# Optimization experiments

Measured on AMD Instinct MI355X. Metric: run time of the kernel, lower is better.

## Reference

```python
import jax, jax.numpy as jnp
import numpy as np

B, N, F_IN, H, MH, STEPS = 8192, 9, 15, 128, 256, 4
E_PER = 16
MASK_IDX = jnp.arange(8)  # mask = [True]*8 + [False]


def setup_inputs() -> dict:
    key = jax.random.key(0)
    ks = jax.random.split(key, 24)
    s = 0.05
    inp = {
        "obs": jax.random.normal(ks[0], (B, 135), jnp.float32),
        "edges": jax.random.randint(ks[1], (B, 2, E_PER), 0, N, jnp.int32),
        "enc_W": jax.random.normal(ks[2], (F_IN, H), jnp.float32) * s,
        "enc_b": jax.random.normal(ks[3], (H,), jnp.float32) * s,
        "msg_W1": jax.random.normal(ks[4], (STEPS, 2 * H, MH), jnp.float32) * s,
        "msg_b1": jax.random.normal(ks[5], (STEPS, MH), jnp.float32) * s,
        "msg_W2": jax.random.normal(ks[6], (STEPS, MH, MH), jnp.float32) * s,
        "msg_b2": jax.random.normal(ks[7], (STEPS, MH), jnp.float32) * s,
        "msg_W3": jax.random.normal(ks[8], (STEPS, MH, H), jnp.float32) * s,
        "msg_b3": jax.random.normal(ks[9], (STEPS, H), jnp.float32) * s,
        "gru_Wi": jax.random.normal(ks[10], (STEPS, H, 3 * H), jnp.float32) * s,
        "gru_Wh": jax.random.normal(ks[11], (STEPS, H, 3 * H), jnp.float32) * s,
        "gru_bi": jax.random.normal(ks[12], (STEPS, 3 * H), jnp.float32) * s,
        "gru_bh": jax.random.normal(ks[13], (STEPS, 3 * H), jnp.float32) * s,
        "dec_W1": jax.random.normal(ks[14], (H, MH), jnp.float32) * s,
        "dec_b1": jax.random.normal(ks[15], (MH,), jnp.float32) * s,
        "dec_W2": jax.random.normal(ks[16], (MH, MH), jnp.float32) * s,
        "dec_b2": jax.random.normal(ks[17], (MH,), jnp.float32) * s,
        "dec_W3": jax.random.normal(ks[18], (MH, 1), jnp.float32) * s,
        "dec_b3": jax.random.normal(ks[19], (1,), jnp.float32) * s,
    }
    return inp


def reference(obs, edges, enc_W, enc_b, msg_W1, msg_b1, msg_W2, msg_b2,
              msg_W3, msg_b3, gru_Wi, gru_Wh, gru_bi, gru_bh,
              dec_W1, dec_b1, dec_W2, dec_b2, dec_W3, dec_b3):
    BN = B * N
    x = obs.reshape(BN, F_IN)                       # [B*N, 15]
    x = jnp.tanh(x @ enc_W + enc_b)                 # encoder -> [B*N, H]

    # flatten per-graph edges into a global edge list, then add self-loops
    offsets = (jnp.arange(B, dtype=jnp.int32) * N)[:, None, None]
    eg = edges + offsets                            # [B, 2, 16]
    loops = jnp.arange(BN, dtype=jnp.int32)
    src = jnp.concatenate([eg[:, 0, :].reshape(-1), loops])  # x_j (source)
    dst = jnp.concatenate([eg[:, 1, :].reshape(-1), loops])  # x_i (target)
    deg = jax.ops.segment_sum(jnp.ones_like(dst, dtype=x.dtype), dst,
                              num_segments=BN)      # >=1 due to self-loops

    for s in range(STEPS):
        m = jnp.concatenate([x[dst], x[src]], axis=-1)       # [E, 2H]
        m = jnp.tanh(m @ msg_W1[s] + msg_b1[s])
        m = jnp.tanh(m @ msg_W2[s] + msg_b2[s])
        m = m @ msg_W3[s] + msg_b3[s]                        # [E, H]
        aggr = jax.ops.segment_sum(m, dst, num_segments=BN) / deg[:, None]
        # GRUCell(input=aggr, hidden=x), PyTorch gate order (r, z, n)
        gi = aggr @ gru_Wi[s] + gru_bi[s]
        gh = x @ gru_Wh[s] + gru_bh[s]
        ir, iz, inn = jnp.split(gi, 3, axis=-1)
        hr, hz, hn = jnp.split(gh, 3, axis=-1)
        r = jax.nn.sigmoid(ir + hr)
        z = jax.nn.sigmoid(iz + hz)
        n = jnp.tanh(inn + r * hn)
        x = (1.0 - z) * n + z * x

    d = jnp.tanh(x @ dec_W1 + dec_b1)
    d = jnp.tanh(d @ dec_W2 + dec_b2)
    d = d @ dec_W3 + dec_b3                                  # [B*N, 1]
    out = d.reshape(B, N)
    return out[:, MASK_IDX]                                  # [B, 8]
```

## Files before the change

### kernel.cpp

```cpp
#include <hip/hip_runtime.h>
#include <hip/hip_bf16.h>
#include <math.h>

#define BGR   8192
#define NND   9
#define BN    73728
#define NE    131072
#define ETOT  204800
#define H     128
#define MH    256
#define FIN   15

typedef __bf16 bf16_t;
typedef bf16_t bf16x8 __attribute__((ext_vector_type(8)));
typedef float  f32x4  __attribute__((ext_vector_type(4)));
typedef float  f32x16 __attribute__((ext_vector_type(16)));

__device__ __forceinline__ unsigned short f2bf(float f) {
    unsigned int u = __float_as_uint(f);
    u += 0x7fff + ((u >> 16) & 1);
    return (unsigned short)(u >> 16);
}
__device__ __forceinline__ unsigned int pkbf(float a, float b) {
    union { __hip_bfloat162 h; unsigned int u; } un;
    un.h = __float22bfloat162_rn(make_float2(a, b));
    return un.u;
}
__device__ __forceinline__ bf16x8 as_frag(int4 v) {
    union { int4 i; bf16x8 f; } u; u.i = v; return u.f;
}
__device__ __forceinline__ float fast_tanh(float v) {
    float e = __expf(2.0f * v);
    return 1.0f - __fdividef(2.0f, e + 1.0f);
}
__device__ __forceinline__ int sw16(int m, int k) {
    return m * 256 + ((((k >> 3) ^ (m & 15)) << 3) | (k & 7));
}
__device__ __forceinline__ int sw_off(int m, int k) {
    return m * 256 + ((((k >> 3) ^ (m & 7)) << 3) | (k & 7));
}

__global__ void deg_kernel(const int* __restrict__ edges, float* __restrict__ inv_deg) {
    int g = blockIdx.x * 256 + threadIdx.x;
    if (g >= BGR) return;
    int cnt[NND];
#pragma unroll
    for (int n = 0; n < NND; ++n) cnt[n] = 1;
    for (int j = 0; j < 16; ++j) {
        int d = edges[g * 32 + 16 + j];
#pragma unroll
        for (int n = 0; n < NND; ++n) cnt[n] += (d == n) ? 1 : 0;
    }
#pragma unroll
    for (int n = 0; n < NND; ++n) inv_deg[g * NND + n] = 1.0f / (float)cnt[n];
}

__global__ void enc_kernel(const float* __restrict__ obs, const float* __restrict__ W,
                           const float* __restrict__ b, float* __restrict__ x) {
    int tid = blockIdx.x * 256 + threadIdx.x;
    int i = tid >> 7, h = tid & 127;
    float acc = b[h];
#pragma unroll
    for (int k = 0; k < FIN; ++k) acc += obs[i * FIN + k] * W[k * H + h];
    x[i * H + h] = tanhf(acc);
}

__global__ void wt_kernel(const float* __restrict__ W1, const float* __restrict__ W2,
                          const float* __restrict__ W3, const float* __restrict__ Wi,
                          const float* __restrict__ Wh, const float* __restrict__ dW1,
                          const float* __restrict__ dW2, unsigned short* __restrict__ out) {
    int idx = blockIdx.x * 256 + threadIdx.x;
    float v;
    if (idx < 262144) {
        int s = idx >> 16, r = idx & 65535, n = r >> 8, k = r & 255;
        v = W1[(s << 16) + (k << 8) + n];
    } else if (idx < 524288) {
        int i2 = idx - 262144;
        int s = i2 >> 16, r = i2 & 65535, n = r >> 8, k = r & 255;
        v = W2[(s << 16) + (k << 8) + n];
    } else if (idx < 655360) {
        int i3 = idx - 524288;
        int s = i3 >> 15, r = i3 & 32767, n = r >> 8, k = r & 255;
        v = W3[(s << 15) + (k << 7) + n];
    } else if (idx < 1179648) {
        int i4 = idx - 655360;
        int s = i4 >> 17, rr = i4 & 131071;
        int p = rr >> 8, k = rr & 255;
        int w = p >> 6, rem = p & 63;
        int gate = rem >> 4, c = rem & 15;
        int h = w * 16 + c;
        const int sb = s * 49152;
        if (gate == 0)      v = (k < 128) ? Wi[sb + k * 384 + h]       : Wh[sb + (k - 128) * 384 + h];
        else if (gate == 1) v = (k < 128) ? Wi[sb + k * 384 + 128 + h] : Wh[sb + (k - 128) * 384 + 128 + h];
        else if (gate == 2) v = (k < 128) ? Wi[sb + k * 384 + 256 + h] : 0.f;
        else                v = (k < 128) ? 0.f                        : Wh[sb + (k - 128) * 384 + 256 + h];
    } else if (idx < 1212416) {
        int i5 = idx - 1179648;
        int n = i5 >> 7, k = i5 & 127;
        v = dW1[k * 256 + n];
    } else {
        int i6 = idx - 1212416;
        int n = i6 >> 8, k = i6 & 255;
        v = dW2[k * 256 + n];
    }
    out[idx] = f2bf(v);
}

__global__ __launch_bounds__(512, 4) void msg_mfma(
        const float* __restrict__ x, const int* __restrict__ edges,
        const unsigned short* __restrict__ W1T, const float* __restrict__ b1,
        const unsigned short* __restrict__ W2T, const float* __restrict__ b2,
        const unsigned short* __restrict__ W3T,
        float* __restrict__ aggr) {
    __shared__ unsigned short bufA[64 * 256];
    __shared__ unsigned short bufB[64 * 256];
    __shared__ int sdst[64];
    const int t  = threadIdx.x;
    const int e0 = blockIdx.x * 64;
    const int wv = t >> 6;
    const int ln = t & 63;
    const int l31 = ln & 31;
    const int lh  = ln >> 5;

    if (t < 64) {
        const int eg = e0 + t;
        sdst[t] = (eg < NE) ? ((eg >> 4) * NND + edges[(eg >> 4) * 32 + 16 + (eg & 15)])
                            : (eg - NE);
    }
    {
        const int row  = t >> 2;
        const int q    = t & 3;
        const int e    = row & 63;
        const int side = row >> 6;
        const int eg   = e0 + e;
        int node;
        if (eg < NE) {
            int g = eg >> 4, j = eg & 15;
            node = g * NND + (side ? edges[g * 32 + j] : edges[g * 32 + 16 + j]);
        } else {
            node = eg - NE;
        }
        const float* xs = x + (size_t)node * H + q * 32;
        const int kbase = side * 128 + q * 32;
#pragma unroll
        for (int i = 0; i < 8; ++i) {
            float4 v = *(const float4*)(xs + i * 4);
            uint2 o;
            o.x = pkbf(v.x, v.y); o.y = pkbf(v.z, v.w);
            *(uint2*)(bufA + sw16(e, kbase + i * 4)) = o;
        }
    }
    __syncthreads();

    {
        f32x16 acc0, acc1;
#pragma unroll
        for (int i = 0; i < 16; ++i) { acc0[i] = 0.f; acc1[i] = 0.f; }
        const unsigned short* wp = W1T + (size_t)(wv * 32 + l31) * 256 + lh * 8;
#pragma unroll
        for (int ks = 0; ks < 16; ++ks) {
            const int kk = ks * 16 + lh * 8;
            bf16x8 a0 = as_frag(*(const int4*)(bufA + sw16(l31, kk)));
            bf16x8 a1 = as_frag(*(const int4*)(bufA + sw16(32 + l31, kk)));
            bf16x8 bw = as_frag(*(const int4*)(wp + ks * 16));
            acc0 = __builtin_amdgcn_mfma_f32_32x32x16_bf16(a0, bw, acc0, 0, 0, 0);
            acc1 = __builtin_amdgcn_mfma_f32_32x32x16_bf16(a1, bw, acc1, 0, 0, 0);
        }
        const int n = wv * 32 + l31;
        const float bias = b1[n];
#pragma unroll
        for (int reg = 0; reg < 16; ++reg) {
            const int mrow = (reg & 3) + ((reg >> 2) << 3) + (lh << 2);
            bufB[sw16(mrow, n)]      = f2bf(fast_tanh(acc0[reg] + bias));
            bufB[sw16(32 + mrow, n)] = f2bf(fast_tanh(acc1[reg] + bias));
        }
    }
    __syncthreads();

    {
        f32x16 acc0, acc1;
#pragma unroll
        for (int i = 0; i < 16; ++i) { acc0[i] = 0.f; acc1[i] = 0.f; }
        const unsigned short* wp = W2T + (size_t)(wv * 32 + l31) * 256 + lh * 8;
#pragma unroll
        for (int ks = 0; ks < 16; ++ks) {
            const int kk = ks * 16 + lh * 8;
            bf16x8 a0 = as_frag(*(const int4*)(bufB + sw16(l31, kk)));
            bf16x8 a1 = as_frag(*(const int4*)(bufB + sw16(32 + l31, kk)));
            bf16x8 bw = as_frag(*(const int4*)(wp + ks * 16));
            acc0 = __builtin_amdgcn_mfma_f32_32x32x16_bf16(a0, bw, acc0, 0, 0, 0);
            acc1 = __builtin_amdgcn_mfma_f32_32x32x16_bf16(a1, bw, acc1, 0, 0, 0);
        }
        const int n = wv * 32 + l31;
        const float bias = b2[n];
#pragma unroll
        for (int reg = 0; reg < 16; ++reg) {
            const int mrow = (reg & 3) + ((reg >> 2) << 3) + (lh << 2);
            bufA[sw16(mrow, n)]      = f2bf(fast_tanh(acc0[reg] + bias));
            bufA[sw16(32 + mrow, n)] = f2bf(fast_tanh(acc1[reg] + bias));
        }
    }
    __syncthreads();

    {
        const int mt = wv & 1, nq = wv >> 1;
        const int n = nq * 32 + l31;
        f32x16 acc;
#pragma unroll
        for (int i = 0; i < 16; ++i) acc[i] = 0.f;
        const unsigned short* wp = W3T + (size_t)n * 256 + lh * 8;
#pragma unroll
        for (int ks = 0; ks < 16; ++ks) {
            const int kk = ks * 16 + lh * 8;
            bf16x8 a = as_frag(*(const int4*)(bufA + sw16(mt * 32 + l31, kk)));
            bf16x8 bw = as_frag(*(const int4*)(wp + ks * 16));
            acc = __builtin_amdgcn_mfma_f32_32x32x16_bf16(a, bw, acc, 0, 0, 0);
        }
#pragma unroll
        for (int reg = 0; reg < 16; ++reg) {
            const int m = mt * 32 + (reg & 3) + ((reg >> 2) << 3) + (lh << 2);
            atomicAdd(aggr + (size_t)sdst[m] * H + n, acc[reg]);
        }
    }
}

__global__ __launch_bounds__(512, 4) void gru_mfma(
        float* __restrict__ x, float* __restrict__ aggr, const float* __restrict__ inv_deg,
        const unsigned short* __restrict__ WG, const float* __restrict__ b3m,
        const float* __restrict__ bi, const float* __restrict__ bh) {
    __shared__ unsigned short bufA[64 * 256];
    const int t = threadIdx.x;
    const int n0 = blockIdx.x * 64;
    const int wv = t >> 6, ln = t & 63, lrow = ln & 15, lq = ln >> 4;

    {
        const int m = t >> 3;
        const int q = t & 7;
        const int k0 = q * 32;
        const int node = n0 + m;
        if (q < 4) {
            const float scale = inv_deg[node];
            const float* src = aggr + (size_t)node * H + k0;
#pragma unroll
            for (int i = 0; i < 8; ++i) {
                float4 v = *(const float4*)(src + i * 4);
                const float4 bb = *(const float4*)(b3m + k0 + i * 4);
                v.x = v.x * scale + bb.x; v.y = v.y * scale + bb.y;
                v.z = v.z * scale + bb.z; v.w = v.w * scale + bb.w;
                uint2 o; o.x = pkbf(v.x, v.y); o.y = pkbf(v.z, v.w);
                *(uint2*)(bufA + sw_off(m, k0 + i * 4)) = o;
            }
        } else {
            const float* src = x + (size_t)node * H + (k0 - 128);
#pragma unroll
            for (int i = 0; i < 8; ++i) {
                float4 v = *(const float4*)(src + i * 4);
                uint2 o; o.x = pkbf(v.x, v.y); o.y = pkbf(v.z, v.w);
                *(uint2*)(bufA + sw_off(m, k0 + i * 4)) = o;
            }
        }
    }
    __syncthreads();

    const f32x4 zero = {0.f, 0.f, 0.f, 0.f};
    f32x4 acc[4][4];
#pragma unroll
    for (int i = 0; i < 4; ++i)
#pragma unroll
        for (int j = 0; j < 4; ++j) acc[i][j] = zero;

    const unsigned short* wgp = WG + (size_t)(wv * 64 + lrow) * 256;
#pragma unroll
    for (int kq = 0; kq < 8; ++kq) {
        const int ko = kq * 32 + lq * 8;
        bf16x8 af[4], bfr[4];
#pragma unroll
        for (int tm = 0; tm < 4; ++tm)
            af[tm] = as_frag(*(const int4*)(bufA + sw_off(tm * 16 + lrow, ko)));
#pragma unroll
        for (int g = 0; g < 4; ++g)
            bfr[g] = as_frag(*(const int4*)(wgp + (size_t)g * 16 * 256 + ko));
#pragma unroll
        for (int tm = 0; tm < 4; ++tm)
#pragma unroll
            for (int g = 0; g < 4; ++g)
                acc[tm][g] = __builtin_amdgcn_mfma_f32_16x16x32_bf16(af[tm], bfr[g], acc[tm][g], 0, 0, 0);
    }

    {
        const int h = wv * 16 + lrow;
        const float b_r = bi[h] + bh[h];
        const float b_z = bi[128 + h] + bh[128 + h];
        const float b_n = bi[256 + h];
        const float b_h = bh[256 + h];
#pragma unroll
        for (int tm = 0; tm < 4; ++tm) {
#pragma unroll
            for (int r = 0; r < 4; ++r) {
                const int node = n0 + tm * 16 + lq * 4 + r;
                const float irhr = acc[tm][0][r] + b_r;
                const float izhz = acc[tm][1][r] + b_z;
                const float inn  = acc[tm][2][r] + b_n;
                const float hn   = acc[tm][3][r] + b_h;
                const float rg = 1.f / (1.f + expf(-irhr));
                const float zg = 1.f / (1.f + expf(-izhz));
                const float ng = tanhf(inn + rg * hn);
                const float xo = x[(size_t)node * H + h];
                x[(size_t)node * H + h] = (1.f - zg) * ng + zg * xo;
                aggr[(size_t)node * H + h] = 0.f;
            }
        }
    }
}

__global__ __launch_bounds__(256, 4) void dec_mfma(
        const float* __restrict__ x,
        const unsigned short* __restrict__ W1T, const float* __restrict__ b1,
        const unsigned short* __restrict__ W2T, const float* __restrict__ b2,
        const float* __restrict__ W3, const float* __restrict__ b3,
        float* __restrict__ out) {
    __shared__ unsigned short buf[64 * 256];
    const int t = threadIdx.x;
    const int id0 = blockIdx.x * 64;
    const int wv = t >> 6, ln = t & 63, lrow = ln & 15, lq = ln >> 4;
    const int nbase = wv * 64;

    {
        const int m = t >> 2, q = t & 3;
        const int id = id0 + m;
        const int node = (id >> 3) * NND + (id & 7);
        const float* src = x + (size_t)node * H + q * 32;
#pragma unroll
        for (int i = 0; i < 8; ++i) {
            float4 v = *(const float4*)(src + i * 4);
            uint2 o; o.x = pkbf(v.x, v.y); o.y = pkbf(v.z, v.w);
            *(uint2*)(buf + sw_off(m, q * 32 + i * 4)) = o;
        }
    }
    __syncthreads();

    const f32x4 zero = {0.f, 0.f, 0.f, 0.f};

    {
        f32x4 acc[4][4];
#pragma unroll
        for (int i = 0; i < 4; ++i)
#pragma unroll
            for (int j = 0; j < 4; ++j) acc[i][j] = zero;
#pragma unroll
        for (int kq = 0; kq < 4; ++kq) {
            const int ko = kq * 32 + lq * 8;
            bf16x8 af[4], bfr[4];
#pragma unroll
            for (int tm = 0; tm < 4; ++tm)
                af[tm] = as_frag(*(const int4*)(buf + sw_off(tm * 16 + lrow, ko)));
#pragma unroll
            for (int tn = 0; tn < 4; ++tn)
                bfr[tn] = as_frag(*(const int4*)(W1T + (size_t)(nbase + tn * 16 + lrow) * 128 + ko));
#pragma unroll
            for (int tm = 0; tm < 4; ++tm)
#pragma unroll
                for (int tn = 0; tn < 4; ++tn)
                    acc[tm][tn] = __builtin_amdgcn_mfma_f32_16x16x32_bf16(af[tm], bfr[tn], acc[tm][tn], 0, 0, 0);
        }
        __syncthreads();
#pragma unroll
        for (int tn = 0; tn < 4; ++tn) {
            const int n = nbase + tn * 16 + lrow;
            const float bias = b1[n];
#pragma unroll
            for (int tm = 0; tm < 4; ++tm)
#pragma unroll
                for (int r = 0; r < 4; ++r) {
                    const int m = tm * 16 + lq * 4 + r;
                    buf[sw_off(m, n)] = f2bf(fast_tanh(acc[tm][tn][r] + bias));
                }
        }
    }
    __syncthreads();

    {
        f32x4 acc[4][4];
#pragma unroll
        for (int i = 0; i < 4; ++i)
#pragma unroll
            for (int j = 0; j < 4; ++j) acc[i][j] = zero;
#pragma unroll
        for (int kq = 0; kq < 8; ++kq) {
            const int ko = kq * 32 + lq * 8;
            bf16x8 af[4], bfr[4];
#pragma unroll
            for (int tm = 0; tm < 4; ++tm)
                af[tm] = as_frag(*(const int4*)(buf + sw_off(tm * 16 + lrow, ko)));
#pragma unroll
            for (int tn = 0; tn < 4; ++tn)
                bfr[tn] = as_frag(*(const int4*)(W2T + (size_t)(nbase + tn * 16 + lrow) * 256 + ko));
#pragma unroll
            for (int tm = 0; tm < 4; ++tm)
#pragma unroll
                for (int tn = 0; tn < 4; ++tn)
                    acc[tm][tn] = __builtin_amdgcn_mfma_f32_16x16x32_bf16(af[tm], bfr[tn], acc[tm][tn], 0, 0, 0);
        }
        __syncthreads();
#pragma unroll
        for (int tn = 0; tn < 4; ++tn) {
            const int n = nbase + tn * 16 + lrow;
            const float bias = b2[n];
#pragma unroll
            for (int tm = 0; tm < 4; ++tm)
#pragma unroll
                for (int r = 0; r < 4; ++r) {
                    const int m = tm * 16 + lq * 4 + r;
                    buf[sw_off(m, n)] = f2bf(fast_tanh(acc[tm][tn][r] + bias));
                }
        }
    }
    __syncthreads();

    {
        const int m = t >> 2, p = t & 3;
        float s = 0.f;
#pragma unroll
        for (int i = 0; i < 64; ++i) {
            const int k = p * 64 + i;
            const float a = __uint_as_float((unsigned int)buf[sw_off(m, k)] << 16);
            s += a * W3[k];
        }
        s += __shfl_xor(s, 1);
        s += __shfl_xor(s, 2);
        if (p == 0) out[id0 + m] = s + b3[0];
    }
}

extern "C" void kernel_launch(void* const* d_in, const int* in_sizes, int n_in,
                              void* d_out, int out_size, void* d_ws, size_t ws_size,
                              hipStream_t stream) {
    const float* obs    = (const float*)d_in[0];
    const int*   edges  = (const int*)  d_in[1];
    const float* enc_W  = (const float*)d_in[2];
    const float* enc_b  = (const float*)d_in[3];
    const float* msg_W1 = (const float*)d_in[4];
    const float* msg_b1 = (const float*)d_in[5];
    const float* msg_W2 = (const float*)d_in[6];
    const float* msg_b2 = (const float*)d_in[7];
    const float* msg_W3 = (const float*)d_in[8];
    const float* msg_b3 = (const float*)d_in[9];
    const float* gru_Wi = (const float*)d_in[10];
    const float* gru_Wh = (const float*)d_in[11];
    const float* gru_bi = (const float*)d_in[12];
    const float* gru_bh = (const float*)d_in[13];
    const float* dec_W1 = (const float*)d_in[14];
    const float* dec_b1 = (const float*)d_in[15];
    const float* dec_W2 = (const float*)d_in[16];
    const float* dec_b2 = (const float*)d_in[17];
    const float* dec_W3 = (const float*)d_in[18];
    const float* dec_b3 = (const float*)d_in[19];

    float* x       = (float*)d_ws;
    float* aggr    = x + (size_t)BN * H;
    float* inv_deg = aggr + (size_t)BN * H;
    unsigned short* wbf = (unsigned short*)(inv_deg + BN);

    hipMemsetAsync(aggr, 0, (size_t)BN * H * sizeof(float), stream);
    deg_kernel<<<(BGR + 255) / 256, 256, 0, stream>>>(edges, inv_deg);
    wt_kernel<<<1277952 / 256, 256, 0, stream>>>(msg_W1, msg_W2, msg_W3, gru_Wi, gru_Wh,
                                                 dec_W1, dec_W2, wbf);
    enc_kernel<<<BN * H / 256, 256, 0, stream>>>(obs, enc_W, enc_b, x);

    for (int s = 0; s < 4; ++s) {
        const unsigned short* W1T = wbf + (size_t)s * 65536;
        const unsigned short* W2T = wbf + 262144 + (size_t)s * 65536;
        const unsigned short* W3T = wbf + 524288 + (size_t)s * 32768;
        const unsigned short* WGs = wbf + 655360 + (size_t)s * 131072;
        msg_mfma<<<ETOT / 64, 512, 0, stream>>>(
            x, edges,
            W1T, msg_b1 + (size_t)s * 256,
            W2T, msg_b2 + (size_t)s * 256,
            W3T,
            aggr);
        gru_mfma<<<BN / 64, 512, 0, stream>>>(
            x, aggr, inv_deg, WGs, msg_b3 + (size_t)s * 128,
            gru_bi + (size_t)s * 384, gru_bh + (size_t)s * 384);
    }

    dec_mfma<<<BGR * 8 / 64, 256, 0, stream>>>(
        x, wbf + 1179648, dec_b1, wbf + 1212416, dec_b2, dec_W3, dec_b3, (float*)d_out);
}
```

Baseline: 1.340 ms.

## Precompute per-node first-layer projections before edge gather in message MLP

The first message layer concat(x_dst, x_src) @ W1 is split into per-node projections x@W1_top and x@W1_bot. A new proj_mfma kernel computes them once per node (73,728 nodes rather than 204,800 edges) and stores them in bf16. msg_mfma then gathers the two projections, adds them with the bias, applies tanh, and runs only the second and third layers. This removes about a third of the edge-level MFMA work, at the cost of an extra kernel launch, a bf16 intermediate buffer written and read per step, and extra rounding on the pre-activation.

Measured after the change: 1.351 ms. About the same (+0.8%).

```diff
diff --git a/kernel.cpp b/kernel.cpp
--- a/kernel.cpp
+++ b/kernel.cpp
@@ -35,6 +35,9 @@
 }
 __device__ __forceinline__ int sw16(int m, int k) {
     return m * 256 + ((((k >> 3) ^ (m & 15)) << 3) | (k & 7));
+}
+__device__ __forceinline__ int swp(int m, int k) {
+    return m * 128 + ((((k >> 3) ^ (m & 15)) << 3) | (k & 7));
 }
 __device__ __forceinline__ int sw_off(int m, int k) {
     return m * 256 + ((((k >> 3) ^ (m & 7)) << 3) | (k & 7));
@@ -98,17 +101,80 @@
         int i5 = idx - 1179648;
         int n = i5 >> 7, k = i5 & 127;
         v = dW1[k * 256 + n];
-    } else {
+    } else if (idx < 1277952) {
         int i6 = idx - 1212416;
         int n = i6 >> 8, k = i6 & 255;
         v = dW2[k * 256 + n];
+    } else {
+        int i7 = idx - 1277952;
+        int s = i7 >> 16, rr = i7 & 65535;
+        int n = rr >> 7, k = rr & 127;
+        v = (n < 256) ? W1[(s << 16) + (k << 8) + n]
+                      : W1[(s << 16) + ((k + 128) << 8) + (n - 256)];
     }
     out[idx] = f2bf(v);
 }
 
+__global__ __launch_bounds__(512, 4) void proj_mfma(
+        const float* __restrict__ x, const unsigned short* __restrict__ W1P,
+        unsigned short* __restrict__ P) {
+    __shared__ unsigned short lbuf[64 * 128];
+    const int t = threadIdx.x;
+    const int n0 = blockIdx.x * 64;
+    const int wv = t >> 6, ln = t & 63, l31 = ln & 31, lh = ln >> 5;
+
+    {
+        const int m = t >> 3, q = t & 7;
+        const float* xs = x + (size_t)(n0 + m) * H + q * 16;
+#pragma unroll
+        for (int i = 0; i < 4; ++i) {
+            float4 v = *(const float4*)(xs + i * 4);
+            uint2 o; o.x = pkbf(v.x, v.y); o.y = pkbf(v.z, v.w);
+            *(uint2*)(lbuf + swp(m, q * 16 + i * 4)) = o;
+        }
+    }
+    __syncthreads();
+
+    f32x16 acc[2][2];
+#pragma unroll
+    for (int a = 0; a < 2; ++a)
+#pragma unroll
+        for (int b = 0; b < 2; ++b)
+#pragma unroll
+            for (int i = 0; i < 16; ++i) acc[a][b][i] = 0.f;
+
+    const int nb = wv * 64;
+    const unsigned short* wp0 = W1P + (size_t)(nb + l31) * 128 + lh * 8;
+    const unsigned short* wp1 = W1P + (size_t)(nb + 32 + l31) * 128 + lh * 8;
+#pragma unroll
+    for (int ks = 0; ks < 8; ++ks) {
+        const int kk = ks * 16 + lh * 8;
+        bf16x8 a0 = as_frag(*(const int4*)(lbuf + swp(l31, kk)));
+        bf16x8 a1 = as_frag(*(const int4*)(lbuf + swp(32 + l31, kk)));
+        bf16x8 w0 = as_frag(*(const int4*)(wp0 + ks * 16));
+        bf16x8 w1 = as_frag(*(const int4*)(wp1 + ks * 16));
+        acc[0][0] = __builtin_amdgcn_mfma_f32_32x32x16_bf16(a0, w0, acc[0][0], 0, 0, 0);
+        acc[0][1] = __builtin_amdgcn_mfma_f32_32x32x16_bf16(a0, w1, acc[0][1], 0, 0, 0);
+        acc[1][0] = __builtin_amdgcn_mfma_f32_32x32x16_bf16(a1, w0, acc[1][0], 0, 0, 0);
+        acc[1][1] = __builtin_amdgcn_mfma_f32_32x32x16_bf16(a1, w1, acc[1][1], 0, 0, 0);
+    }
+
+#pragma unroll
+    for (int mt = 0; mt < 2; ++mt)
+#pragma unroll
+        for (int nt = 0; nt < 2; ++nt) {
+            const int col = nb + nt * 32 + l31;
+#pragma unroll
+            for (int reg = 0; reg < 16; ++reg) {
+                const int mrow = mt * 32 + (reg & 3) + ((reg >> 2) << 3) + (lh << 2);
+                P[(size_t)(n0 + mrow) * 512 + col] = f2bf(acc[mt][nt][reg]);
+            }
+        }
+}
+
 __global__ __launch_bounds__(512, 4) void msg_mfma(
-        const float* __restrict__ x, const int* __restrict__ edges,
-        const unsigned short* __restrict__ W1T, const float* __restrict__ b1,
+        const unsigned short* __restrict__ P, const int* __restrict__ edges,
+        const float* __restrict__ b1,
         const unsigned short* __restrict__ W2T, const float* __restrict__ b2,
         const unsigned short* __restrict__ W3T,
         float* __restrict__ aggr) {
@@ -128,26 +194,36 @@
                             : (eg - NE);
     }
     {
-        const int row  = t >> 2;
-        const int q    = t & 3;
-        const int e    = row & 63;
-        const int side = row >> 6;
-        const int eg   = e0 + e;
-        int node;
+        const int row = t >> 3;
+        const int c0  = (t & 7) * 32;
+        const int eg  = e0 + row;
+        int dn, sn;
         if (eg < NE) {
             int g = eg >> 4, j = eg & 15;
-            node = g * NND + (side ? edges[g * 32 + j] : edges[g * 32 + 16 + j]);
+            sn = g * NND + edges[g * 32 + j];
+            dn = g * NND + edges[g * 32 + 16 + j];
         } else {
-            node = eg - NE;
-        }
-        const float* xs = x + (size_t)node * H + q * 32;
-        const int kbase = side * 128 + q * 32;
-#pragma unroll
-        for (int i = 0; i < 8; ++i) {
-            float4 v = *(const float4*)(xs + i * 4);
-            uint2 o;
-            o.x = pkbf(v.x, v.y); o.y = pkbf(v.z, v.w);
-            *(uint2*)(bufA + sw16(e, kbase + i * 4)) = o;
+            dn = sn = eg - NE;
+        }
+        const unsigned short* up = P + (size_t)dn * 512 + c0;
+        const unsigned short* vp = P + (size_t)sn * 512 + 256 + c0;
+#pragma unroll
+        for (int i = 0; i < 4; ++i) {
+            const uint4 uu = *(const uint4*)(up + i * 8);
+            const uint4 vv = *(const uint4*)(vp + i * 8);
+            const unsigned int ua[4] = {uu.x, uu.y, uu.z, uu.w};
+            const unsigned int va[4] = {vv.x, vv.y, vv.z, vv.w};
+            unsigned int op[4];
+#pragma unroll
+            for (int j = 0; j < 4; ++j) {
+                const float2 bb = *(const float2*)(b1 + c0 + i * 8 + j * 2);
+                const float s0 = fast_tanh(__uint_as_float(ua[j] << 16) +
+                                           __uint_as_float(va[j] << 16) + bb.x);
+                const float s1 = fast_tanh(__uint_as_float(ua[j] & 0xffff0000u) +
+                                           __uint_as_float(va[j] & 0xffff0000u) + bb.y);
+                op[j] = pkbf(s0, s1);
+            }
+            *(uint4*)(bufA + sw16(row, c0 + i * 8)) = make_uint4(op[0], op[1], op[2], op[3]);
         }
     }
     __syncthreads();
@@ -156,7 +232,7 @@
         f32x16 acc0, acc1;
 #pragma unroll
         for (int i = 0; i < 16; ++i) { acc0[i] = 0.f; acc1[i] = 0.f; }
-        const unsigned short* wp = W1T + (size_t)(wv * 32 + l31) * 256 + lh * 8;
+        const unsigned short* wp = W2T + (size_t)(wv * 32 + l31) * 256 + lh * 8;
 #pragma unroll
         for (int ks = 0; ks < 16; ++ks) {
             const int kk = ks * 16 + lh * 8;
@@ -167,7 +243,7 @@
             acc1 = __builtin_amdgcn_mfma_f32_32x32x16_bf16(a1, bw, acc1, 0, 0, 0);
         }
         const int n = wv * 32 + l31;
-        const float bias = b1[n];
+        const float bias = b2[n];
 #pragma unroll
         for (int reg = 0; reg < 16; ++reg) {
             const int mrow = (reg & 3) + ((reg >> 2) << 3) + (lh << 2);
@@ -178,31 +254,6 @@
     __syncthreads();
 
     {
-        f32x16 acc0, acc1;
-#pragma unroll
-        for (int i = 0; i < 16; ++i) { acc0[i] = 0.f; acc1[i] = 0.f; }
-        const unsigned short* wp = W2T + (size_t)(wv * 32 + l31) * 256 + lh * 8;
-#pragma unroll
-        for (int ks = 0; ks < 16; ++ks) {
-            const int kk = ks * 16 + lh * 8;
-            bf16x8 a0 = as_frag(*(const int4*)(bufB + sw16(l31, kk)));
-            bf16x8 a1 = as_frag(*(const int4*)(bufB + sw16(32 + l31, kk)));
-            bf16x8 bw = as_frag(*(const int4*)(wp + ks * 16));
-            acc0 = __builtin_amdgcn_mfma_f32_32x32x16_bf16(a0, bw, acc0, 0, 0, 0);
-            acc1 = __builtin_amdgcn_mfma_f32_32x32x16_bf16(a1, bw, acc1, 0, 0, 0);
-        }
-        const int n = wv * 32 + l31;
-        const float bias = b2[n];
-#pragma unroll
-        for (int reg = 0; reg < 16; ++reg) {
-            const int mrow = (reg & 3) + ((reg >> 2) << 3) + (lh << 2);
-            bufA[sw16(mrow, n)]      = f2bf(fast_tanh(acc0[reg] + bias));
-            bufA[sw16(32 + mrow, n)] = f2bf(fast_tanh(acc1[reg] + bias));
-        }
-    }
-    __syncthreads();
-
-    {
         const int mt = wv & 1, nq = wv >> 1;
         const int n = nq * 32 + l31;
         f32x16 acc;
@@ -212,7 +263,7 @@
 #pragma unroll
         for (int ks = 0; ks < 16; ++ks) {
             const int kk = ks * 16 + lh * 8;
-            bf16x8 a = as_frag(*(const int4*)(bufA + sw16(mt * 32 + l31, kk)));
+            bf16x8 a = as_frag(*(const int4*)(bufB + sw16(mt * 32 + l31, kk)));
             bf16x8 bw = as_frag(*(const int4*)(wp + ks * 16));
             acc = __builtin_amdgcn_mfma_f32_32x32x16_bf16(a, bw, acc, 0, 0, 0);
         }
@@ -460,21 +511,23 @@
     float* aggr    = x + (size_t)BN * H;
     float* inv_deg = aggr + (size_t)BN * H;
     unsigned short* wbf = (unsigned short*)(inv_deg + BN);
+    unsigned short* P   = wbf + 1540096;
 
     hipMemsetAsync(aggr, 0, (size_t)BN * H * sizeof(float), stream);
     deg_kernel<<<(BGR + 255) / 256, 256, 0, stream>>>(edges, inv_deg);
-    wt_kernel<<<1277952 / 256, 256, 0, stream>>>(msg_W1, msg_W2, msg_W3, gru_Wi, gru_Wh,
+    wt_kernel<<<1540096 / 256, 256, 0, stream>>>(msg_W1, msg_W2, msg_W3, gru_Wi, gru_Wh,
                                                  dec_W1, dec_W2, wbf);
     enc_kernel<<<BN * H / 256, 256, 0, stream>>>(obs, enc_W, enc_b, x);
 
     for (int s = 0; s < 4; ++s) {
-        const unsigned short* W1T = wbf + (size_t)s * 65536;
         const unsigned short* W2T = wbf + 262144 + (size_t)s * 65536;
         const unsigned short* W3T = wbf + 524288 + (size_t)s * 32768;
         const unsigned short* WGs = wbf + 655360 + (size_t)s * 131072;
+        const unsigned short* W1P = wbf + 1277952 + (size_t)s * 65536;
+        proj_mfma<<<BN / 64, 512, 0, stream>>>(x, W1P, P);
         msg_mfma<<<ETOT / 64, 512, 0, stream>>>(
-            x, edges,
-            W1T, msg_b1 + (size_t)s * 256,
+            P, edges,
+            msg_b1 + (size_t)s * 256,
             W2T, msg_b2 + (size_t)s * 256,
             W3T,
             aggr);
```
